# Kernel tuning notes

Hardware: AMD Instinct MI355X
Metric: run time of the kernel (lower is better)

## Reference

```python
import jax, jax.numpy as jnp
import numpy as np

TAU = 2.0          # spikingjelly LIFNode default
V_TH = 7.0         # from source
DECREASE = 0.5     # decrease_factor
ALPHA = 4.0        # sigmoid surrogate alpha (spikingjelly default)


@jax.custom_vjp
def spike(v):
    # Heaviside with sigmoid surrogate gradient
    return (v >= 0.0).astype(v.dtype)

def _spike_fwd(v):
    return spike(v), v

def _spike_bwd(v, g):
    s = jax.nn.sigmoid(ALPHA * v)
    return (g * ALPHA * s * (1.0 - s),)

spike.defvjp(_spike_fwd, _spike_bwd)


def setup_inputs() -> dict:
    key = jax.random.key(0)
    k1, k2, k3 = jax.random.split(key, 3)
    B, C, T = 4096, 14, 600
    x = jax.random.normal(k1, (B, C, T), dtype=jnp.float32)
    # weights: normal(mean=0.8, std=0.05) clamped to [0,1]; nn.Linear stores [out,in]
    W1 = jnp.clip(0.8 + 0.05 * jax.random.normal(k2, (14, 14), dtype=jnp.float32), 0.0, 1.0)
    W2 = jnp.clip(0.8 + 0.05 * jax.random.normal(k3, (500, 14), dtype=jnp.float32), 0.0, 1.0)
    return {"x": x, "W1": W1, "W2": W2}


def _forward(x, W1, W2):
    B = x.shape[0]
    xt = jnp.transpose(x, (2, 0, 1))  # [T, B, 14]

    v1_0 = jnp.zeros((B, 14), x.dtype)
    v2_0 = jnp.zeros((B, 500), x.dtype)
    cache0 = jnp.zeros((B, 14), x.dtype)

    def step(carry, x_t):
        v1, v2, cache = carry
        # block 1: linear + decayed feedback of previous spikes
        i1 = x_t @ W1.T + DECREASE * cache
        v1 = v1 + (i1 - v1) / TAU          # LIF charge (decay_input, v_reset=0)
        s1 = spike(v1 - V_TH)
        v1 = v1 * (1.0 - s1)               # hard reset to 0
        # block 2
        i2 = s1 @ W2.T
        v2 = v2 + (i2 - v2) / TAU
        s2 = spike(v2 - V_TH)
        v2 = v2 * (1.0 - s2)
        return (v1, v2, s1), None

    (v1, v2, cache), _ = jax.lax.scan(step, (v1_0, v2_0, cache0), xt)
    return jnp.exp(v2)  # liquid state [B, 500]


def reference(x, W1, W2):
    return _forward(x, W1, W2)
```

## Files before the change

kernel.cpp:

```cpp
#include <hip/hip_runtime.h>
#include <math.h>

#define T     600
#define C     14
#define NOUT  500
#define W     128
#define DSTR  132
#define CAP   64

__global__ __launch_bounds__(64, 4)
void snn_v5(const float* __restrict__ x, const float* __restrict__ W1,
            const float* __restrict__ W2, float* __restrict__ out) {
    __shared__ float    ds[15 * DSTR];
    __shared__ unsigned evs[CAP];
    __shared__ int      ecnt;

    const int  lane = threadIdx.x;
    const long row  = blockIdx.x;
    const float* xr = &x[row * (long)(C * T)];

    if (lane == 0) ecnt = 0;
    for (int i = lane; i < DSTR; i += 64) ds[14 * DSTR + i] = 0.f;

    const int ce = (lane < C) ? lane : 14;
    float v1 = 0.f;

    for (int t0 = 0; t0 < T; t0 += W) {
        const int wlen = (T - t0 < W) ? (T - t0) : W;
        __syncthreads();

        if (2 * lane < wlen) {
            const int tt = t0 + 2 * lane;
            float2 xv[C];
            #pragma unroll
            for (int j = 0; j < C; ++j)
                xv[j] = *(const float2*)&xr[j * T + tt];
            #pragma unroll
            for (int c = 0; c < C; ++c) {
                float ax = 0.f, ay = 0.f;
                #pragma unroll
                for (int j = 0; j < C; ++j) {
                    const float wv = 0.5f * W1[c * C + j];
                    ax = fmaf(xv[j].x, wv, ax);
                    ay = fmaf(xv[j].y, wv, ay);
                }
                *(float2*)&ds[c * DSTR + 2 * lane] = make_float2(ax, ay);
            }
        }
        __syncthreads();

        const float* dp = &ds[ce * DSTR];
        for (int q = 0; q < wlen; q += 4) {
            const float4 hd = *(const float4*)&dp[q];
            const float a  = fmaf(v1, 0.5f, hd.x);
            const float b  = fmaf(a,  0.5f, hd.y);
            const float c2 = fmaf(b,  0.5f, hd.z);
            const float d  = fmaf(c2, 0.5f, hd.w);
            const float m  = fmaxf(fmaxf(a, b), fmaxf(c2, d));
            if (__builtin_expect(__ballot(m >= 7.0f) != 0ull, 0)) {
                float vv = v1;
                #pragma unroll
                for (int u = 0; u < 4; ++u) {
                    const float h = (u == 0) ? hd.x : (u == 1) ? hd.y
                                  : (u == 2) ? hd.z : hd.w;
                    vv = fmaf(vv, 0.5f, h);
                    const unsigned mk = (unsigned)__ballot(vv >= 7.0f) & 0x3FFFu;
                    if (mk) {
                        if (vv >= 7.0f) vv = 0.5f;
                        if (lane == 0 && ecnt < CAP)
                            evs[ecnt++] = ((unsigned)(t0 + q + u) << 14) | mk;
                    }
                }
                v1 = vv;
            } else {
                v1 = d;
            }
        }
    }
    __syncthreads();

    const int n = (ecnt < CAP) ? ecnt : CAP;
    float v2[8];
    #pragma unroll
    for (int k = 0; k < 8; ++k) v2[k] = 0.f;
    int tprev = -1;

    for (int e = 0; e < n; ++e) {
        const unsigned ev = evs[e];
        const int t = (int)(ev >> 14);
        unsigned mm = ev & 0x3FFFu;
        float i2[8];
        #pragma unroll
        for (int k = 0; k < 8; ++k) i2[k] = 0.f;
        while (mm) {
            const int c = (int)__builtin_ctz(mm);
            mm &= mm - 1;
            #pragma unroll
            for (int k = 0; k < 8; ++k) {
                const int o = lane + (k << 6);
                if (o < NOUT) i2[k] += W2[o * C + c];
            }
        }
        const int gap = t - tprev - 1;
        if (gap > 0) {
            #pragma unroll
            for (int k = 0; k < 8; ++k) v2[k] = ldexpf(v2[k], -gap);
        }
        #pragma unroll
        for (int k = 0; k < 8; ++k) {
            const float v = v2[k] + (i2[k] - v2[k]) * 0.5f;
            v2[k] = (v >= 7.0f) ? 0.f : v;
        }
        tprev = t;
    }
    {
        const int gap = (T - 1) - tprev;
        if (gap > 0) {
            #pragma unroll
            for (int k = 0; k < 8; ++k) v2[k] = ldexpf(v2[k], -gap);
        }
    }
    #pragma unroll
    for (int k = 0; k < 8; ++k) {
        const int o = lane + (k << 6);
        if (o < NOUT) out[row * NOUT + o] = expf(v2[k]);
    }
}

extern "C" void kernel_launch(void* const* d_in, const int* in_sizes, int n_in,
                              void* d_out, int out_size, void* d_ws, size_t ws_size,
                              hipStream_t stream) {
    const float* x  = (const float*)d_in[0];
    const float* W1 = (const float*)d_in[1];
    const float* W2 = (const float*)d_in[2];
    float* o = (float*)d_out;
    const int B = in_sizes[0] / (C * T);
    snn_v5<<<B, 64, 0, stream>>>(x, W1, W2, o);
}
```

Baseline: 49.15 us.

## Replace serial per-timestep LIF scan with wave-parallel prefix scan over window

Computes layer-1 membrane potentials for each 128-step window with a parallel linear-recurrence prefix scan across lanes, using ds_bpermute with power-of-two decay weights. The serial per-timestep scan from shared memory runs only when a spike threshold might be crossed. It also prefetches the next window's inputs into registers, uses packed fma for the W1 projection, and replaces block barriers with wave barriers. The intent is to cut the long serial dependency chain in the common no-spike case. In exchange it uses more registers, adds a conservative 6.999 threshold check, and relies on the 0.25^k scale factors staying precise for up to 64 lanes.

```diff
diff --git a/kernel.cpp b/kernel.cpp
--- a/kernel.cpp
+++ b/kernel.cpp
@@ -8,76 +8,140 @@
 #define DSTR  132
 #define CAP   64
 
-__global__ __launch_bounds__(64, 4)
-void snn_v5(const float* __restrict__ x, const float* __restrict__ W1,
+typedef float f32x2 __attribute__((ext_vector_type(2)));
+
+__device__ __forceinline__ float bperm(int addr, float v) {
+    return __int_as_float(__builtin_amdgcn_ds_bpermute(addr, __float_as_int(v)));
+}
+__device__ __forceinline__ f32x2 fma2(f32x2 a, f32x2 b, f32x2 c) {
+#if __has_builtin(__builtin_elementwise_fma)
+    return __builtin_elementwise_fma(a, b, c);
+#else
+    f32x2 r; r.x = fmaf(a.x, b.x, c.x); r.y = fmaf(a.y, b.y, c.y); return r;
+#endif
+}
+
+__global__ __launch_bounds__(64)
+void snn_v6(const float* __restrict__ x, const float* __restrict__ W1,
             const float* __restrict__ W2, float* __restrict__ out) {
     __shared__ float    ds[15 * DSTR];
     __shared__ unsigned evs[CAP];
-    __shared__ int      ecnt;
 
     const int  lane = threadIdx.x;
     const long row  = blockIdx.x;
     const float* xr = &x[row * (long)(C * T)];
 
-    if (lane == 0) ecnt = 0;
     for (int i = lane; i < DSTR; i += 64) ds[14 * DSTR + i] = 0.f;
 
-    const int ce = (lane < C) ? lane : 14;
-    float v1 = 0.f;
+    const int   a1 = ((lane - 1) & 63) << 2;
+    const int   a2 = ((lane - 2) & 63) << 2;
+    const int   a4 = ((lane - 4) & 63) << 2;
+    const int   a8 = ((lane - 8) & 63) << 2;
+    const float m1 = (lane >= 1) ? 0.25f            : 0.f;
+    const float m2 = (lane >= 2) ? 0.0625f          : 0.f;
+    const float m4 = (lane >= 4) ? 0.00390625f      : 0.f;
+    const float m8 = (lane >= 8) ? 1.52587890625e-5f: 0.f;
+    const float kl = ldexpf(1.f, -2 * lane - 2);
+
+    float v1s[C];
+    #pragma unroll
+    for (int c = 0; c < C; ++c) v1s[c] = 0.f;
+    int ecnt = 0;
+
+    f32x2 xv[C];
+    #pragma unroll
+    for (int j = 0; j < C; ++j)
+        xv[j] = *(const f32x2*)&xr[j * T + 2 * lane];
 
     for (int t0 = 0; t0 < T; t0 += W) {
         const int wlen = (T - t0 < W) ? (T - t0) : W;
-        __syncthreads();
-
-        if (2 * lane < wlen) {
-            const int tt = t0 + 2 * lane;
-            float2 xv[C];
-            #pragma unroll
-            for (int j = 0; j < C; ++j)
-                xv[j] = *(const float2*)&xr[j * T + tt];
-            #pragma unroll
-            for (int c = 0; c < C; ++c) {
-                float ax = 0.f, ay = 0.f;
-                #pragma unroll
-                for (int j = 0; j < C; ++j) {
-                    const float wv = 0.5f * W1[c * C + j];
-                    ax = fmaf(xv[j].x, wv, ax);
-                    ay = fmaf(xv[j].y, wv, ay);
+
+        f32x2 acc[C];
+        #pragma unroll
+        for (int c = 0; c < C; ++c) {
+            f32x2 a = {0.f, 0.f};
+            #pragma unroll
+            for (int j = 0; j < C; ++j) {
+                const float wv = 0.5f * W1[c * C + j];
+                const f32x2 wvv = {wv, wv};
+                a = fma2(xv[j], wvv, a);
+            }
+            acc[c] = a;
+        }
+        if (t0 + W < T) {
+            const int tn = t0 + W + 2 * lane;
+            #pragma unroll
+            for (int j = 0; j < C; ++j) {
+                const f32x2 z = {0.f, 0.f};
+                xv[j] = (tn + 1 < T) ? *(const f32x2*)&xr[j * T + tn] : z;
+            }
+        }
+
+        bool  anyf = false;
+        float wv_[C];
+        #pragma unroll
+        for (int c = 0; c < C; ++c) {
+            const float de = acc[c].x, dd = acc[c].y;
+            float S = fmaf(de, 0.5f, dd);
+            S = fmaf(bperm(a1, S), m1, S);
+            S = fmaf(bperm(a2, S), m2, S);
+            S = fmaf(bperm(a4, S), m4, S);
+            S = fmaf(bperm(a8, S), m8, S);
+            const float Wv = fmaf(v1s[c], kl, S);
+            float tp = bperm(a1, Wv);
+            tp = (lane == 0) ? v1s[c] : tp;
+            const float ve = fmaf(tp, 0.5f, de);
+            anyf = anyf || (fmaxf(ve, Wv) >= 6.999f);
+            wv_[c] = Wv;
+        }
+        const int lastl = (wlen >> 1) - 1;
+
+        if (__builtin_expect(__ballot(anyf) != 0ull, 0)) {
+            #pragma unroll
+            for (int c = 0; c < C; ++c)
+                *(f32x2*)&ds[c * DSTR + 2 * lane] = acc[c];
+            __builtin_amdgcn_wave_barrier();
+            float vv = 0.f;
+            #pragma unroll
+            for (int c = 0; c < C; ++c) vv = (lane == c) ? v1s[c] : vv;
+            const int ce = (lane < C) ? lane : 14;
+            const float* dp = &ds[ce * DSTR];
+            for (int q = 0; q < wlen; q += 4) {
+                const float4 hd = *(const float4*)&dp[q];
+                const float A  = fmaf(vv, 0.5f, hd.x);
+                const float Bq = fmaf(A,  0.5f, hd.y);
+                const float Cq = fmaf(Bq, 0.5f, hd.z);
+                const float Dq = fmaf(Cq, 0.5f, hd.w);
+                const float Mq = fmaxf(fmaxf(A, Bq), fmaxf(Cq, Dq));
+                if (__ballot(Mq >= 7.0f)) {
+                    float vp = vv;
+                    #pragma unroll
+                    for (int u = 0; u < 4; ++u) {
+                        const float h = (u==0)?hd.x:(u==1)?hd.y:(u==2)?hd.z:hd.w;
+                        vp = fmaf(vp, 0.5f, h);
+                        const unsigned long long bal = __ballot(vp >= 7.0f);
+                        if (bal) {
+                            if (vp >= 7.0f) vp = 0.5f;
+                            if (ecnt < CAP && lane == 0)
+                                evs[ecnt] = ((unsigned)(t0 + q + u) << 14)
+                                          | ((unsigned)bal & 0x3FFFu);
+                            ++ecnt;
+                        }
+                    }
+                    vv = vp;
+                } else {
+                    vv = Dq;
                 }
-                *(float2*)&ds[c * DSTR + 2 * lane] = make_float2(ax, ay);
-            }
-        }
-        __syncthreads();
-
-        const float* dp = &ds[ce * DSTR];
-        for (int q = 0; q < wlen; q += 4) {
-            const float4 hd = *(const float4*)&dp[q];
-            const float a  = fmaf(v1, 0.5f, hd.x);
-            const float b  = fmaf(a,  0.5f, hd.y);
-            const float c2 = fmaf(b,  0.5f, hd.z);
-            const float d  = fmaf(c2, 0.5f, hd.w);
-            const float m  = fmaxf(fmaxf(a, b), fmaxf(c2, d));
-            if (__builtin_expect(__ballot(m >= 7.0f) != 0ull, 0)) {
-                float vv = v1;
-                #pragma unroll
-                for (int u = 0; u < 4; ++u) {
-                    const float h = (u == 0) ? hd.x : (u == 1) ? hd.y
-                                  : (u == 2) ? hd.z : hd.w;
-                    vv = fmaf(vv, 0.5f, h);
-                    const unsigned mk = (unsigned)__ballot(vv >= 7.0f) & 0x3FFFu;
-                    if (mk) {
-                        if (vv >= 7.0f) vv = 0.5f;
-                        if (lane == 0 && ecnt < CAP)
-                            evs[ecnt++] = ((unsigned)(t0 + q + u) << 14) | mk;
-                    }
-                }
-                v1 = vv;
-            } else {
-                v1 = d;
-            }
-        }
-    }
-    __syncthreads();
+            }
+            __builtin_amdgcn_wave_barrier();
+            #pragma unroll
+            for (int c = 0; c < C; ++c) v1s[c] = __shfl(vv, c, 64);
+        } else {
+            #pragma unroll
+            for (int c = 0; c < C; ++c) v1s[c] = __shfl(wv_[c], lastl, 64);
+        }
+    }
+    __builtin_amdgcn_wave_barrier();
 
     const int n = (ecnt < CAP) ? ecnt : CAP;
     float v2[8];
@@ -135,5 +199,5 @@
     const float* W2 = (const float*)d_in[2];
     float* o = (float*)d_out;
     const int B = in_sizes[0] / (C * T);
-    snn_v5<<<B, 64, 0, stream>>>(x, W1, W2, o);
-}
+    snn_v6<<<B, 64, 0, stream>>>(x, W1, W2, o);
+}
```

Measured after the change: 115.5 us. 2.35x slower.

## Prefetch next x window into registers and scan LIF in 16-step blocks

Applied to the files above, without the earlier changes.

Loads the next 128-step window of x into registers while the current window is projected, and drops __syncthreads in favor of explicit LDS waitcnt since the block is a single wavefront. The spike counter becomes a per-lane register, and the scan checks thresholds once per 16 steps with software-prefetched LDS reads, using 4 independent max chains. This is meant to hide global-load latency and cut barrier and ballot overhead. It relies on a 64-thread block being exactly one wave, and it raises register pressure from the extra prefetch buffers.

```diff
diff --git a/kernel.cpp b/kernel.cpp
--- a/kernel.cpp
+++ b/kernel.cpp
@@ -8,76 +8,115 @@
 #define DSTR  132
 #define CAP   64
 
+typedef float f32x2 __attribute__((ext_vector_type(2)));
+
 __global__ __launch_bounds__(64, 4)
-void snn_v5(const float* __restrict__ x, const float* __restrict__ W1,
+void snn_v7(const float* __restrict__ x, const float* __restrict__ W1,
             const float* __restrict__ W2, float* __restrict__ out) {
-    __shared__ float    ds[15 * DSTR];
+    __shared__ float    D[C * DSTR];
     __shared__ unsigned evs[CAP];
-    __shared__ int      ecnt;
 
     const int  lane = threadIdx.x;
     const long row  = blockIdx.x;
     const float* xr = &x[row * (long)(C * T)];
+    const int  ce   = (lane < C) ? lane : (C - 1);
 
-    if (lane == 0) ecnt = 0;
-    for (int i = lane; i < DSTR; i += 64) ds[14 * DSTR + i] = 0.f;
+    f32x2 xv[C];
+    #pragma unroll
+    for (int j = 0; j < C; ++j)
+        xv[j] = *(const f32x2*)&xr[j * T + 2 * lane];
 
-    const int ce = (lane < C) ? lane : 14;
     float v1 = 0.f;
+    int   ecnt = 0;
 
-    for (int t0 = 0; t0 < T; t0 += W) {
-        const int wlen = (T - t0 < W) ? (T - t0) : W;
-        __syncthreads();
+    for (int w = 0; w < 5; ++w) {
+        const int t0 = w * W;
 
-        if (2 * lane < wlen) {
-            const int tt = t0 + 2 * lane;
-            float2 xv[C];
+        f32x2 xh[C];
+        #pragma unroll
+        for (int j = 0; j < C; ++j) xh[j] = xv[j] * 0.5f;
+
+        if (w < 4) {
+            const int tn = t0 + W + 2 * lane;
             #pragma unroll
-            for (int j = 0; j < C; ++j)
-                xv[j] = *(const float2*)&xr[j * T + tt];
-            #pragma unroll
-            for (int c = 0; c < C; ++c) {
-                float ax = 0.f, ay = 0.f;
-                #pragma unroll
-                for (int j = 0; j < C; ++j) {
-                    const float wv = 0.5f * W1[c * C + j];
-                    ax = fmaf(xv[j].x, wv, ax);
-                    ay = fmaf(xv[j].y, wv, ay);
-                }
-                *(float2*)&ds[c * DSTR + 2 * lane] = make_float2(ax, ay);
+            for (int j = 0; j < C; ++j) {
+                const f32x2 z = {0.f, 0.f};
+                xv[j] = (tn + 1 < T) ? *(const f32x2*)&xr[j * T + tn] : z;
             }
         }
-        __syncthreads();
 
-        const float* dp = &ds[ce * DSTR];
-        for (int q = 0; q < wlen; q += 4) {
-            const float4 hd = *(const float4*)&dp[q];
-            const float a  = fmaf(v1, 0.5f, hd.x);
-            const float b  = fmaf(a,  0.5f, hd.y);
-            const float c2 = fmaf(b,  0.5f, hd.z);
-            const float d  = fmaf(c2, 0.5f, hd.w);
-            const float m  = fmaxf(fmaxf(a, b), fmaxf(c2, d));
-            if (__builtin_expect(__ballot(m >= 7.0f) != 0ull, 0)) {
-                float vv = v1;
+        #pragma unroll
+        for (int c = 0; c < C; ++c) {
+            f32x2 a = {0.f, 0.f};
+            #pragma unroll
+            for (int j = 0; j < C; ++j) {
+                const float wv = W1[c * C + j];
+                a.x = fmaf(xh[j].x, wv, a.x);
+                a.y = fmaf(xh[j].y, wv, a.y);
+            }
+            *(f32x2*)&D[c * DSTR + 2 * lane] = a;
+        }
+
+        asm volatile("s_waitcnt lgkmcnt(0)" ::: "memory");
+        __builtin_amdgcn_sched_barrier(0);
+
+        const float* dp = &D[ce * DSTR];
+        const int nb = (w < 4) ? 8 : 6;
+        float4 c0 = *(const float4*)&dp[0];
+        float4 c1 = *(const float4*)&dp[4];
+        float4 c2 = *(const float4*)&dp[8];
+        float4 c3 = *(const float4*)&dp[12];
+        for (int b = 0; b < nb; ++b) {
+            float4 n0, n1, n2, n3;
+            const bool more = (b + 1 < nb);
+            if (more) {
+                const float* np_ = dp + 16 * (b + 1);
+                n0 = *(const float4*)&np_[0];
+                n1 = *(const float4*)&np_[4];
+                n2 = *(const float4*)&np_[8];
+                n3 = *(const float4*)&np_[12];
+            }
+            float h[16];
+            h[0]=c0.x; h[1]=c0.y; h[2]=c0.z; h[3]=c0.w;
+            h[4]=c1.x; h[5]=c1.y; h[6]=c1.z; h[7]=c1.w;
+            h[8]=c2.x; h[9]=c2.y; h[10]=c2.z; h[11]=c2.w;
+            h[12]=c3.x; h[13]=c3.y; h[14]=c3.z; h[15]=c3.w;
+
+            float vv = v1;
+            float m0 = -1e30f, m1 = -1e30f, m2 = -1e30f, m3 = -1e30f;
+            #pragma unroll
+            for (int u = 0; u < 16; u += 4) {
+                vv = fmaf(vv, 0.5f, h[u]);     m0 = fmaxf(m0, vv);
+                vv = fmaf(vv, 0.5f, h[u + 1]); m1 = fmaxf(m1, vv);
+                vv = fmaf(vv, 0.5f, h[u + 2]); m2 = fmaxf(m2, vv);
+                vv = fmaf(vv, 0.5f, h[u + 3]); m3 = fmaxf(m3, vv);
+            }
+            const float mx = fmaxf(fmaxf(m0, m1), fmaxf(m2, m3));
+
+            if (__builtin_expect(__ballot(mx >= 7.0f) != 0ull, 0)) {
+                float vp = v1;
                 #pragma unroll
-                for (int u = 0; u < 4; ++u) {
-                    const float h = (u == 0) ? hd.x : (u == 1) ? hd.y
-                                  : (u == 2) ? hd.z : hd.w;
-                    vv = fmaf(vv, 0.5f, h);
-                    const unsigned mk = (unsigned)__ballot(vv >= 7.0f) & 0x3FFFu;
-                    if (mk) {
-                        if (vv >= 7.0f) vv = 0.5f;
+                for (int u = 0; u < 16; ++u) {
+                    vp = fmaf(vp, 0.5f, h[u]);
+                    const unsigned long long bal = __ballot(vp >= 7.0f);
+                    if (bal) {
+                        if (vp >= 7.0f) vp = 0.5f;
                         if (lane == 0 && ecnt < CAP)
-                            evs[ecnt++] = ((unsigned)(t0 + q + u) << 14) | mk;
+                            evs[ecnt] = ((unsigned)(t0 + 16 * b + u) << 14)
+                                      | ((unsigned)bal & 0x3FFFu);
+                        ++ecnt;
                     }
                 }
+                v1 = vp;
+            } else {
                 v1 = vv;
-            } else {
-                v1 = d;
             }
+            if (more) { c0 = n0; c1 = n1; c2 = n2; c3 = n3; }
         }
     }
-    __syncthreads();
+
+    asm volatile("s_waitcnt lgkmcnt(0)" ::: "memory");
+    __builtin_amdgcn_sched_barrier(0);
 
     const int n = (ecnt < CAP) ? ecnt : CAP;
     float v2[8];
@@ -135,5 +174,5 @@
     const float* W2 = (const float*)d_in[2];
     float* o = (float*)d_out;
     const int B = in_sizes[0] / (C * T);
-    snn_v5<<<B, 64, 0, stream>>>(x, W1, W2, o);
+    snn_v7<<<B, 64, 0, stream>>>(x, W1, W2, o);
 }
```

Result: slower. 57.26 us (+16.5%).

## Software-pipeline W1 projection with double-buffered LDS and 16-step batched LIF scan

Applied to the files above, without the earlier changes.

Replaces the windowed synchronous loop with a fully unrolled, double-buffered pipeline. The next window's x loads and W1 projection are interleaved into the serial LIF recurrence, so the latency-bound scan overlaps with memory and FMA work. Projections now use packed 2-wide FMAs with unscaled weights, and the threshold scale changes accordingly (14, reset 1). The scan checks thresholds once per 16 steps and falls back to a noinline replay function, and __syncthreads is dropped because each wave handles its own row. The cost is much higher register pressure (28 f32x2 x-registers plus prefetch), the occupancy hint is removed, and the hardcoded T-specific unrolling is fragile.

```diff
diff --git a/kernel.cpp b/kernel.cpp
--- a/kernel.cpp
+++ b/kernel.cpp
@@ -8,76 +8,171 @@
 #define DSTR  132
 #define CAP   64
 
-__global__ __launch_bounds__(64, 4)
-void snn_v5(const float* __restrict__ x, const float* __restrict__ W1,
-            const float* __restrict__ W2, float* __restrict__ out) {
-    __shared__ float    ds[15 * DSTR];
+typedef float f32x2 __attribute__((ext_vector_type(2)));
+
+__device__ __forceinline__ f32x2 fma2(f32x2 a, f32x2 b, f32x2 c) {
+#if __has_builtin(__builtin_elementwise_fma)
+    return __builtin_elementwise_fma(a, b, c);
+#else
+    f32x2 r; r.x = fmaf(a.x, b.x, c.x); r.y = fmaf(a.y, b.y, c.y); return r;
+#endif
+}
+__device__ __forceinline__ f32x2 wp(float w) { f32x2 r; r.x = w; r.y = w; return r; }
+
+struct SR { float u; int e; };
+
+__device__ __noinline__ SR slow_replay(float u, float4 h0, float4 h1, float4 h2,
+                                       float4 h3, int tb, int lane, int ecnt,
+                                       unsigned* evp) {
+    float h[16] = {h0.x,h0.y,h0.z,h0.w, h1.x,h1.y,h1.z,h1.w,
+                   h2.x,h2.y,h2.z,h2.w, h3.x,h3.y,h3.z,h3.w};
+    #pragma unroll
+    for (int i = 0; i < 16; ++i) {
+        u = fmaf(u, 0.5f, h[i]);
+        const unsigned long long bal = __ballot(u >= 14.0f);
+        if (bal) {
+            if (u >= 14.0f) u = 1.0f;
+            if (lane == 0 && ecnt < CAP)
+                evp[ecnt] = ((unsigned)(tb + i) << 14) | ((unsigned)bal & 0x3FFFu);
+            ++ecnt;
+        }
+    }
+    SR r; r.u = u; r.e = ecnt; return r;
+}
+
+#define REP14(M) M(0) M(1) M(2) M(3) M(4) M(5) M(6) M(7) M(8) M(9) M(10) M(11) M(12) M(13)
+#define DECLA(j) f32x2 A##j;
+#define DECLB(j) f32x2 B##j;
+#define LDA0(j)  A##j = *(const f32x2*)&xr[(j)*T + tpa];
+#define LDB1(j)  B##j = *(const f32x2*)&xr[(j)*T + tpb];
+#define ZEROA(j) A##j = zz;
+#define AJ(j) A##j
+#define BJ(j) B##j
+
+#define GEMM_C(SJ, cc, DB) { \
+  f32x2 a_ = {0.f, 0.f}; \
+  a_ = fma2(SJ(0),  wp(W1g[(cc)*14+0]),  a_); \
+  a_ = fma2(SJ(1),  wp(W1g[(cc)*14+1]),  a_); \
+  a_ = fma2(SJ(2),  wp(W1g[(cc)*14+2]),  a_); \
+  a_ = fma2(SJ(3),  wp(W1g[(cc)*14+3]),  a_); \
+  a_ = fma2(SJ(4),  wp(W1g[(cc)*14+4]),  a_); \
+  a_ = fma2(SJ(5),  wp(W1g[(cc)*14+5]),  a_); \
+  a_ = fma2(SJ(6),  wp(W1g[(cc)*14+6]),  a_); \
+  a_ = fma2(SJ(7),  wp(W1g[(cc)*14+7]),  a_); \
+  a_ = fma2(SJ(8),  wp(W1g[(cc)*14+8]),  a_); \
+  a_ = fma2(SJ(9),  wp(W1g[(cc)*14+9]),  a_); \
+  a_ = fma2(SJ(10), wp(W1g[(cc)*14+10]), a_); \
+  a_ = fma2(SJ(11), wp(W1g[(cc)*14+11]), a_); \
+  a_ = fma2(SJ(12), wp(W1g[(cc)*14+12]), a_); \
+  a_ = fma2(SJ(13), wp(W1g[(cc)*14+13]), a_); \
+  *(f32x2*)&(DB)[(cc)*DSTR + 2*lane] = a_; }
+
+#define CHB(TB, NP) { \
+  const float* np_ = (NP); \
+  const float4 n0_ = *(const float4*)&np_[0]; \
+  const float4 n1_ = *(const float4*)&np_[4]; \
+  const float4 n2_ = *(const float4*)&np_[8]; \
+  const float4 n3_ = *(const float4*)&np_[12]; \
+  float vv = u, m0, m1, m2, m3; \
+  vv = fmaf(vv, 0.5f, c0.x); m0 = vv; \
+  vv = fmaf(vv, 0.5f, c0.y); m1 = vv; \
+  vv = fmaf(vv, 0.5f, c0.z); m2 = vv; \
+  vv = fmaf(vv, 0.5f, c0.w); m3 = vv; \
+  vv = fmaf(vv, 0.5f, c1.x); m0 = fmaxf(m0, vv); \
+  vv = fmaf(vv, 0.5f, c1.y); m1 = fmaxf(m1, vv); \
+  vv = fmaf(vv, 0.5f, c1.z); m2 = fmaxf(m2, vv); \
+  vv = fmaf(vv, 0.5f, c1.w); m3 = fmaxf(m3, vv); \
+  vv = fmaf(vv, 0.5f, c2.x); m0 = fmaxf(m0, vv); \
+  vv = fmaf(vv, 0.5f, c2.y); m1 = fmaxf(m1, vv); \
+  vv = fmaf(vv, 0.5f, c2.z); m2 = fmaxf(m2, vv); \
+  vv = fmaf(vv, 0.5f, c2.w); m3 = fmaxf(m3, vv); \
+  vv = fmaf(vv, 0.5f, c3.x); m0 = fmaxf(m0, vv); \
+  vv = fmaf(vv, 0.5f, c3.y); m1 = fmaxf(m1, vv); \
+  vv = fmaf(vv, 0.5f, c3.z); m2 = fmaxf(m2, vv); \
+  vv = fmaf(vv, 0.5f, c3.w); m3 = fmaxf(m3, vv); \
+  const float mx_ = fmaxf(fmaxf(m0, m1), fmaxf(m2, m3)); \
+  if (__builtin_expect(__ballot(mx_ >= 14.0f) != 0ull, 0)) { \
+    const SR r_ = slow_replay(u, c0, c1, c2, c3, (TB), lane, ecnt, (unsigned*)evs); \
+    u = r_.u; ecnt = r_.e; \
+  } else { u = vv; } \
+  c0 = n0_; c1 = n1_; c2 = n2_; c3 = n3_; }
+
+#define FH_BATCH(b, j0, j1) \
+  CHB(tA + 16*(b), dp0 + 16*((b)+1)); \
+  A##j0 = *(const f32x2*)&xr[(j0)*T + tn1]; \
+  A##j1 = *(const f32x2*)&xr[(j1)*T + tn1]; \
+  GEMM_C(BJ, j0, db1); \
+  GEMM_C(BJ, j1, db1);
+
+#define SH_BATCH(b, j0, j1) \
+  CHB(tB + 16*(b), dp1 + 16*((b)+1)); \
+  if (i == 0) { \
+    B##j0 = *(const f32x2*)&xr[(j0)*T + tn2]; \
+    B##j1 = *(const f32x2*)&xr[(j1)*T + tn2]; \
+  } \
+  GEMM_C(AJ, j0, db0); \
+  GEMM_C(AJ, j1, db0);
+
+__global__ __launch_bounds__(64)
+void snn_v11(const float* __restrict__ x, const float* __restrict__ W1g,
+             const float* __restrict__ W2, float* __restrict__ out) {
+    __shared__ float    db0[C * DSTR];
+    __shared__ float    db1[C * DSTR];
     __shared__ unsigned evs[CAP];
-    __shared__ int      ecnt;
 
     const int  lane = threadIdx.x;
     const long row  = blockIdx.x;
     const float* xr = &x[row * (long)(C * T)];
-
-    if (lane == 0) ecnt = 0;
-    for (int i = lane; i < DSTR; i += 64) ds[14 * DSTR + i] = 0.f;
-
-    const int ce = (lane < C) ? lane : 14;
-    float v1 = 0.f;
-
-    for (int t0 = 0; t0 < T; t0 += W) {
-        const int wlen = (T - t0 < W) ? (T - t0) : W;
-        __syncthreads();
-
-        if (2 * lane < wlen) {
-            const int tt = t0 + 2 * lane;
-            float2 xv[C];
-            #pragma unroll
-            for (int j = 0; j < C; ++j)
-                xv[j] = *(const float2*)&xr[j * T + tt];
-            #pragma unroll
-            for (int c = 0; c < C; ++c) {
-                float ax = 0.f, ay = 0.f;
-                #pragma unroll
-                for (int j = 0; j < C; ++j) {
-                    const float wv = 0.5f * W1[c * C + j];
-                    ax = fmaf(xv[j].x, wv, ax);
-                    ay = fmaf(xv[j].y, wv, ay);
-                }
-                *(float2*)&ds[c * DSTR + 2 * lane] = make_float2(ax, ay);
-            }
-        }
-        __syncthreads();
-
-        const float* dp = &ds[ce * DSTR];
-        for (int q = 0; q < wlen; q += 4) {
-            const float4 hd = *(const float4*)&dp[q];
-            const float a  = fmaf(v1, 0.5f, hd.x);
-            const float b  = fmaf(a,  0.5f, hd.y);
-            const float c2 = fmaf(b,  0.5f, hd.z);
-            const float d  = fmaf(c2, 0.5f, hd.w);
-            const float m  = fmaxf(fmaxf(a, b), fmaxf(c2, d));
-            if (__builtin_expect(__ballot(m >= 7.0f) != 0ull, 0)) {
-                float vv = v1;
-                #pragma unroll
-                for (int u = 0; u < 4; ++u) {
-                    const float h = (u == 0) ? hd.x : (u == 1) ? hd.y
-                                  : (u == 2) ? hd.z : hd.w;
-                    vv = fmaf(vv, 0.5f, h);
-                    const unsigned mk = (unsigned)__ballot(vv >= 7.0f) & 0x3FFFu;
-                    if (mk) {
-                        if (vv >= 7.0f) vv = 0.5f;
-                        if (lane == 0 && ecnt < CAP)
-                            evs[ecnt++] = ((unsigned)(t0 + q + u) << 14) | mk;
-                    }
-                }
-                v1 = vv;
-            } else {
-                v1 = d;
-            }
-        }
-    }
-    __syncthreads();
+    const int  ce   = (lane < C) ? lane : (C - 1);
+
+    REP14(DECLA)
+    REP14(DECLB)
+
+    { const int tpa = 2 * lane; REP14(LDA0) }
+    GEMM_C(AJ, 0, db0)  GEMM_C(AJ, 1, db0)  GEMM_C(AJ, 2, db0)
+    GEMM_C(AJ, 3, db0)  GEMM_C(AJ, 4, db0)  GEMM_C(AJ, 5, db0)
+    GEMM_C(AJ, 6, db0)  GEMM_C(AJ, 7, db0)  GEMM_C(AJ, 8, db0)
+    GEMM_C(AJ, 9, db0)  GEMM_C(AJ, 10, db0) GEMM_C(AJ, 11, db0)
+    GEMM_C(AJ, 12, db0) GEMM_C(AJ, 13, db0)
+    { const int tpb = W + 2 * lane; REP14(LDB1) }
+
+    float u = 0.f;
+    int   ecnt = 0;
+    const float* dp0 = &db0[ce * DSTR];
+    const float* dp1 = &db1[ce * DSTR];
+    float4 c0 = *(const float4*)&dp0[0];
+    float4 c1 = *(const float4*)&dp0[4];
+    float4 c2 = *(const float4*)&dp0[8];
+    float4 c3 = *(const float4*)&dp0[12];
+
+    for (int i = 0; i < 2; ++i) {
+        const int tA = (2 * i) * W;
+        const int tB = (2 * i + 1) * W;
+        int tn1 = (2 * i + 2) * W + 2 * lane;
+        if (tn1 > T - 2) tn1 = T - 2;
+        const int tn2 = 3 * W + 2 * lane;
+
+        FH_BATCH(0, 0, 1)   FH_BATCH(1, 2, 3)   FH_BATCH(2, 4, 5)
+        FH_BATCH(3, 6, 7)   FH_BATCH(4, 8, 9)   FH_BATCH(5, 10, 11)
+        FH_BATCH(6, 12, 13)
+        CHB(tA + 112, dp1)
+
+        if (i == 1 && lane >= (T - 4 * W) / 2) {
+            const f32x2 zz = {0.f, 0.f};
+            REP14(ZEROA)
+        }
+        SH_BATCH(0, 0, 1)   SH_BATCH(1, 2, 3)   SH_BATCH(2, 4, 5)
+        SH_BATCH(3, 6, 7)   SH_BATCH(4, 8, 9)   SH_BATCH(5, 10, 11)
+        SH_BATCH(6, 12, 13)
+        CHB(tB + 112, dp0)
+    }
+
+    CHB(512 + 0,  dp0 + 16)
+    CHB(512 + 16, dp0 + 32)
+    CHB(512 + 32, dp0 + 48)
+    CHB(512 + 48, dp0 + 64)
+    CHB(512 + 64, dp0 + 80)
+    CHB(512 + 80, dp0)
 
     const int n = (ecnt < CAP) ? ecnt : CAP;
     float v2[8];
@@ -135,5 +230,5 @@
     const float* W2 = (const float*)d_in[2];
     float* o = (float*)d_out;
     const int B = in_sizes[0] / (C * T);
-    snn_v5<<<B, 64, 0, stream>>>(x, W1, W2, o);
-}
+    snn_v11<<<B, 64, 0, stream>>>(x, W1, W2, o);
+}
```

Measured after the change: 68.81 us. 1.4x slower.
